# Performance work log

Hardware: AMD Instinct MI355X
Metric: run time of the kernel (lower is better)

Reference implementation:

```python
import jax, jax.numpy as jnp
import numpy as np

H, DK = 8, 32
D_MODEL = H * DK  # 256
Q_DIM = K_DIM = V_DIM = 256
B, T, S = 4, 4, 1024
NEG = -1e10


def setup_inputs() -> dict:
    rng = jax.random.key(0)
    ks = jax.random.split(rng, 12)
    w = lambda k, shp: (jax.random.normal(k, shp, jnp.float32) * 0.02)
    return {
        "query": jax.random.normal(ks[0], (B, T, S, Q_DIM), jnp.float32),
        "key": jax.random.normal(ks[1], (B, T, S, K_DIM), jnp.float32),
        "value": jax.random.normal(ks[2], (B, T, S, V_DIM), jnp.float32),
        "mask": jax.random.randint(ks[3], (B, T), 1, S + 1),  # valid lengths in [1, S]
        "Wq": w(ks[4], (D_MODEL, Q_DIM)), "bq": jnp.zeros((D_MODEL,), jnp.float32),
        "Wk": w(ks[5], (D_MODEL, K_DIM)), "bk": jnp.zeros((D_MODEL,), jnp.float32),
        "Wv": w(ks[6], (D_MODEL, V_DIM)), "bv": jnp.zeros((D_MODEL,), jnp.float32),
        "Wo": w(ks[7], (Q_DIM, D_MODEL)), "bo": jnp.zeros((Q_DIM,), jnp.float32),
    }


def reference(query, key, value, mask, Wq, bq, Wk, bk, Wv, bv, Wo, bo):
    b, t, s, _ = query.shape
    # projections -> [B,T,h,S,d_k]
    def proj(x, W, bias):
        y = jnp.einsum('btsf,df->btsd', x, W) + bias
        return y.reshape(b, t, s, H, DK).transpose(0, 1, 3, 2, 4)
    q = proj(query, Wq, bq)
    k = proj(key, Wk, bk)
    v = proj(value, Wv, bv)
    # scores [B,T,h,S,S]
    scores = jnp.einsum('bthqd,bthkd->bthqk', q, k) / jnp.sqrt(jnp.float32(DK))
    # vectorized length mask: positions < len on both axes (replaces torch python loop)
    valid = jnp.arange(s)[None, None, :] < mask[:, :, None]        # [B,T,S]
    m = valid[:, :, None, :, None] & valid[:, :, None, None, :]    # [B,T,1,S,S]
    scores = jnp.where(m, scores, NEG)
    p = jax.nn.softmax(scores, axis=-1)
    x = jnp.einsum('bthqk,bthkd->bthqd', p, v)                     # [B,T,h,S,d_k]
    x = x.transpose(0, 1, 3, 2, 4).reshape(b, t, s, H * DK)
    return jnp.einsum('btsd,qd->btsq', x, Wo) + bo
```

## Files before the change

kernel.cpp:

```cpp
#include <hip/hip_runtime.h>

#define EXPC 0.25505654442163f

typedef __attribute__((ext_vector_type(8))) short bfrag;
typedef __attribute__((ext_vector_type(4))) float ffrag;
typedef __attribute__((ext_vector_type(8))) unsigned int u8v;
typedef __attribute__((ext_vector_type(4))) unsigned int u4v;
typedef __attribute__((ext_vector_type(2))) unsigned int u2v;

__device__ __forceinline__ short f2bf(float x) {
  union { float f; unsigned u; } v; v.f = x;
  return (short)((v.u + 0x8000u) >> 16);
}

__device__ __forceinline__ unsigned int packbf(float a, float b) {
  return __builtin_amdgcn_perm(__float_as_uint(b) + 0x8000u,
                               __float_as_uint(a) + 0x8000u, 0x07060302u);
}

__device__ __forceinline__ bfrag cvtp(u8v x) {
  u4v r;
#pragma unroll
  for (int i = 0; i < 4; ++i)
    r[i] = __builtin_amdgcn_perm(x[2 * i + 1] + 0x8000u, x[2 * i] + 0x8000u, 0x07060302u);
  union { u4v u; bfrag b; } c; c.u = r; return c.b;
}
__device__ __forceinline__ bfrag cvt8(const float* __restrict__ p) {
  return cvtp(*(const u8v*)p);
}

__global__ __launch_bounds__(256, 4) void proj_kv(
    const float* __restrict__ kin, const float* __restrict__ Wk,
    const float* __restrict__ bk, const float* __restrict__ vin,
    const float* __restrict__ Wv, const float* __restrict__ bv,
    short* __restrict__ ko, short* __restrict__ vt) {
  const int t = threadIdx.x;
  const int lane = t & 63, wid = t >> 6;
  const int lrow = lane & 15, lq = lane >> 4;
  __shared__ __align__(16) char lds[18432];
  const int row4 = t >> 2, c4 = (t & 3) * 8;

  const bool isK = blockIdx.x < 512;
  if (isK) {
    const int bx = blockIdx.x >> 1, d0 = (blockIdx.x & 1) * 128;
    const int m0 = bx * 64;
    short* Ab = (short*)lds;
    short* Bb = (short*)(lds + 5120);
    short* tile = (short*)lds;
    ffrag acc[4][2] = {};
    u8v pa, pb0, pb1;
    pa  = *(const u8v*)(kin + (size_t)(m0 + row4) * 256 + c4);
    pb0 = *(const u8v*)(Wk + (size_t)(d0 + row4) * 256 + c4);
    pb1 = *(const u8v*)(Wk + (size_t)(d0 + 64 + row4) * 256 + c4);
    *(bfrag*)(Ab + row4 * 40 + c4) = cvtp(pa);
    *(bfrag*)(Bb + row4 * 40 + c4) = cvtp(pb0);
    *(bfrag*)(Bb + (64 + row4) * 40 + c4) = cvtp(pb1);
#pragma unroll 1
    for (int s = 0; s < 8; ++s) {
      __syncthreads();
      if (s < 7) {
        const int k1 = (s + 1) * 32;
        pa  = *(const u8v*)(kin + (size_t)(m0 + row4) * 256 + k1 + c4);
        pb0 = *(const u8v*)(Wk + (size_t)(d0 + row4) * 256 + k1 + c4);
        pb1 = *(const u8v*)(Wk + (size_t)(d0 + 64 + row4) * 256 + k1 + c4);
      }
      bfrag a[4], b[2];
#pragma unroll
      for (int i = 0; i < 4; ++i)
        a[i] = *(const bfrag*)(Ab + (i * 16 + lrow) * 40 + lq * 8);
#pragma unroll
      for (int j = 0; j < 2; ++j)
        b[j] = *(const bfrag*)(Bb + (wid * 32 + j * 16 + lrow) * 40 + lq * 8);
#pragma unroll
      for (int i = 0; i < 4; ++i)
#pragma unroll
        for (int j = 0; j < 2; ++j)
          acc[i][j] = __builtin_amdgcn_mfma_f32_16x16x32_bf16(a[i], b[j], acc[i][j], 0, 0, 0);
      __syncthreads();
      if (s < 7) {
        *(bfrag*)(Ab + row4 * 40 + c4) = cvtp(pa);
        *(bfrag*)(Bb + row4 * 40 + c4) = cvtp(pb0);
        *(bfrag*)(Bb + (64 + row4) * 40 + c4) = cvtp(pb1);
      }
    }
    __syncthreads();
#pragma unroll
    for (int j = 0; j < 2; ++j) {
      int dl = wid * 32 + j * 16 + lrow;
      float bs = bk[d0 + dl];
#pragma unroll
      for (int i = 0; i < 4; ++i)
#pragma unroll
        for (int r = 0; r < 4; ++r)
          tile[(i * 16 + lq * 4 + r) * 136 + dl] = f2bf(acc[i][j][r] + bs);
    }
    __syncthreads();
#pragma unroll
    for (int p = 0; p < 4; ++p) {
      int id2 = p * 256 + t;
      int row = id2 >> 4, c = id2 & 15;
      bfrag v = *(const bfrag*)(tile + row * 136 + c * 8);
      *(bfrag*)(ko + (size_t)(m0 + row) * 256 + d0 + c * 8) = v;
    }
  } else {
    const int t2 = blockIdx.x - 512;
    const int bx = t2 >> 1, d0 = (t2 & 1) * 128;
    const int n0 = bx * 64;
    short* Aw = (short*)lds;
    short* Bv = (short*)(lds + 10240);
    short* tile = (short*)lds;
    ffrag acc[2][4] = {};
    u8v pv, pw0, pw1;
    pw0 = *(const u8v*)(Wv + (size_t)(d0 + row4) * 256 + c4);
    pw1 = *(const u8v*)(Wv + (size_t)(d0 + 64 + row4) * 256 + c4);
    pv  = *(const u8v*)(vin + (size_t)(n0 + row4) * 256 + c4);
    *(bfrag*)(Aw + row4 * 40 + c4) = cvtp(pw0);
    *(bfrag*)(Aw + (64 + row4) * 40 + c4) = cvtp(pw1);
    *(bfrag*)(Bv + row4 * 40 + c4) = cvtp(pv);
#pragma unroll 1
    for (int s = 0; s < 8; ++s) {
      __syncthreads();
      if (s < 7) {
        const int k1 = (s + 1) * 32;
        pw0 = *(const u8v*)(Wv + (size_t)(d0 + row4) * 256 + k1 + c4);
        pw1 = *(const u8v*)(Wv + (size_t)(d0 + 64 + row4) * 256 + k1 + c4);
        pv  = *(const u8v*)(vin + (size_t)(n0 + row4) * 256 + k1 + c4);
      }
      bfrag a[2], b[4];
#pragma unroll
      for (int i = 0; i < 2; ++i)
        a[i] = *(const bfrag*)(Aw + (wid * 32 + i * 16 + lrow) * 40 + lq * 8);
#pragma unroll
      for (int j = 0; j < 4; ++j)
        b[j] = *(const bfrag*)(Bv + (j * 16 + lrow) * 40 + lq * 8);
#pragma unroll
      for (int i = 0; i < 2; ++i)
#pragma unroll
        for (int j = 0; j < 4; ++j)
          acc[i][j] = __builtin_amdgcn_mfma_f32_16x16x32_bf16(a[i], b[j], acc[i][j], 0, 0, 0);
      __syncthreads();
      if (s < 7) {
        *(bfrag*)(Aw + row4 * 40 + c4) = cvtp(pw0);
        *(bfrag*)(Aw + (64 + row4) * 40 + c4) = cvtp(pw1);
        *(bfrag*)(Bv + row4 * 40 + c4) = cvtp(pv);
      }
    }
    __syncthreads();
#pragma unroll
    for (int i = 0; i < 2; ++i)
#pragma unroll
      for (int r = 0; r < 4; ++r) {
        int dl = wid * 32 + i * 16 + lq * 4 + r;
        float bs = bv[d0 + dl];
#pragma unroll
        for (int j = 0; j < 4; ++j)
          tile[dl * 72 + j * 16 + lrow] = f2bf(acc[i][j][r] + bs);
      }
    __syncthreads();
    const int bt = n0 >> 10, sl0 = n0 & 1023;
#pragma unroll
    for (int p = 0; p < 4; ++p) {
      int id2 = p * 256 + t;
      int dl = id2 >> 3, c = id2 & 7;
      bfrag v = *(const bfrag*)(tile + dl * 72 + c * 8);
      *(bfrag*)(vt + (size_t)bt * 262144 + (size_t)(d0 + dl) * 1024 + sl0 + c * 8) = v;
    }
  }
}

__global__ __launch_bounds__(512, 4) void attn_fused(
    const float* __restrict__ query, const float* __restrict__ Wq,
    const float* __restrict__ bq, const float* __restrict__ Wo,
    const float* __restrict__ bo, const short* __restrict__ K,
    const short* __restrict__ Vt, const int* __restrict__ mask,
    float* __restrict__ out) {
  const int lane = threadIdx.x & 63, wid = threadIdx.x >> 6;
  const int lrow = lane & 15, lq = lane >> 4;
  const int id = blockIdx.x;
  const int bt = (id + (id >> 8)) & 15;
  const int qt = id >> 4;
  const int q0 = qt * 32;
  const int L = mask[bt];
  const int h = wid;
  const bool isLast = (qt == 31);
  const int nvalid = min(max(L - q0, 0), 32);

  if (nvalid <= 0 && !isLast) return;
  const bool colsumOnly = isLast && (nvalid <= 0);

  __shared__ __align__(16) short qx[32 * 264];
  __shared__ __align__(16) unsigned int ptbuf[8][16 * 36];
  unsigned int* ptg = &ptbuf[wid][0];
  float* vbuf = (float*)&ptbuf[0][0];

  const short* Vb = Vt + ((size_t)bt * 8 + h) * 32768;
  float l_i[2];
  ffrag o[2][2] = {};

  if (!colsumOnly) {
    {
      const int n0 = h * 32;
      const float* X = query + ((size_t)bt * 1024 + q0) * 256;
      ffrag acc[2][2] = {};
      u8v xa[2], wb[2], xa_n[2], wb_n[2];
#pragma unroll
      for (int i = 0; i < 2; ++i)
        xa[i] = *(const u8v*)(X + (size_t)(i * 16 + lrow) * 256 + lq * 8);
#pragma unroll
      for (int j = 0; j < 2; ++j)
        wb[j] = *(const u8v*)(Wq + (size_t)(n0 + j * 16 + lrow) * 256 + lq * 8);
#pragma unroll 1
      for (int tt = 0; tt < 8; ++tt) {
        if (tt < 7) {
          const int kk = (tt + 1) * 32;
#pragma unroll
          for (int i = 0; i < 2; ++i)
            xa_n[i] = *(const u8v*)(X + (size_t)(i * 16 + lrow) * 256 + kk + lq * 8);
#pragma unroll
          for (int j = 0; j < 2; ++j)
            wb_n[j] = *(const u8v*)(Wq + (size_t)(n0 + j * 16 + lrow) * 256 + kk + lq * 8);
        }
        bfrag a[2], b[2];
#pragma unroll
        for (int i = 0; i < 2; ++i) a[i] = cvtp(xa[i]);
#pragma unroll
        for (int j = 0; j < 2; ++j) b[j] = cvtp(wb[j]);
#pragma unroll
        for (int i = 0; i < 2; ++i)
#pragma unroll
          for (int j = 0; j < 2; ++j)
            acc[i][j] = __builtin_amdgcn_mfma_f32_16x16x32_bf16(a[i], b[j], acc[i][j], 0, 0, 0);
#pragma unroll
        for (int i = 0; i < 2; ++i) xa[i] = xa_n[i];
#pragma unroll
        for (int j = 0; j < 2; ++j) wb[j] = wb_n[j];
      }
#pragma unroll
      for (int j = 0; j < 2; ++j) {
        int d = n0 + j * 16 + lrow;
        float bs = bq[d];
#pragma unroll
        for (int i = 0; i < 2; ++i)
#pragma unroll
          for (int r = 0; r < 4; ++r)
            qx[(i * 16 + lq * 4 + r) * 264 + d] = f2bf((acc[i][j][r] + bs) * EXPC);
      }
    }

    const short* Kb = K + (size_t)bt * 262144;
    bfrag qf[2];
#pragma unroll
    for (int g = 0; g < 2; ++g)
      qf[g] = *(const bfrag*)(qx + (g * 16 + lrow) * 264 + h * 32 + lq * 8);

    const int nchunk = (L + 63) >> 6;
    float l_loc[2] = {0.f, 0.f};
    bfrag kf[4], kf_n[4];
#pragma unroll
    for (int f = 0; f < 4; ++f)
      kf[f] = *(const bfrag*)(Kb + (size_t)(f * 16 + lrow) * 256 + h * 32 + lq * 8);

#pragma unroll 1
    for (int c = 0; c < nchunk; ++c) {
      const int kc = c * 64;
      const ffrag zf = {0.f, 0.f, 0.f, 0.f};
      if (c + 1 < nchunk) {
#pragma unroll
        for (int f = 0; f < 4; ++f)
          kf_n[f] = *(const bfrag*)(Kb + (size_t)(kc + 64 + f * 16 + lrow) * 256 + h * 32 + lq * 8);
      }
      bfrag av[2][2];
#pragma unroll
      for (int dj = 0; dj < 2; ++dj)
#pragma unroll
        for (int b = 0; b < 2; ++b)
          av[dj][b] = *(const bfrag*)(Vb + (size_t)(dj * 16 + lrow) * 1024 + kc + b * 32 + lq * 8);

      ffrag st[2][4];
#pragma unroll
      for (int g = 0; g < 2; ++g)
#pragma unroll
        for (int f = 0; f < 4; ++f)
          st[g][f] = __builtin_amdgcn_mfma_f32_16x16x32_bf16(kf[f], qf[g], zf, 0, 0, 0);

      const bool fullc = (kc + 64 <= L);
#pragma unroll
      for (int g = 0; g < 2; ++g) {
        float p[4][4];
        if (fullc) {
#pragma unroll
          for (int f = 0; f < 4; ++f)
#pragma unroll
            for (int r = 0; r < 4; ++r) {
              p[f][r] = __builtin_amdgcn_exp2f(st[g][f][r]);
              l_loc[g] += p[f][r];
            }
        } else {
#pragma unroll
          for (int f = 0; f < 4; ++f)
#pragma unroll
            for (int r = 0; r < 4; ++r) {
              int kr = kc + f * 16 + lq * 4 + r;
              float pv = (kr < L) ? __builtin_amdgcn_exp2f(st[g][f][r]) : 0.f;
              p[f][r] = pv;
              l_loc[g] += pv;
            }
        }
#pragma unroll
        for (int f = 0; f < 4; ++f) {
          u2v w;
          w[0] = packbf(p[f][0], p[f][1]);
          w[1] = packbf(p[f][2], p[f][3]);
          *(u2v*)(ptg + lrow * 36 + 8 * f + 2 * lq) = w;
        }
#pragma unroll
        for (int b = 0; b < 2; ++b) {
          u4v pv = *(const u4v*)(ptg + lrow * 36 + 16 * b + 4 * lq);
          union { u4v u; bfrag bf; } pt; pt.u = pv;
#pragma unroll
          for (int dj = 0; dj < 2; ++dj)
            o[g][dj] = __builtin_amdgcn_mfma_f32_16x16x32_bf16(av[dj][b], pt.bf, o[g][dj], 0, 0, 0);
        }
      }
#pragma unroll
      for (int f = 0; f < 4; ++f) kf[f] = kf_n[f];
    }

#pragma unroll
    for (int g = 0; g < 2; ++g) {
      float rs = l_loc[g];
      rs += __shfl_xor(rs, 16);
      rs += __shfl_xor(rs, 32);
      l_i[g] = rs;
    }
  } else {
#pragma unroll
    for (int g = 0; g < 2; ++g) l_i[g] = 1024.f;
  }

  if (isLast && nvalid < 32) {
#pragma unroll
    for (int g = 0; g < 2; ++g) {
      bool inv = (g * 16 + lrow) >= nvalid;
      if (inv) {
        l_i[g] = 1024.f;
#pragma unroll
        for (int dj = 0; dj < 2; ++dj)
#pragma unroll
          for (int r = 0; r < 4; ++r) o[g][dj][r] = 0.f;
      }
    }
    bfrag ind[2];
#pragma unroll
    for (int g = 0; g < 2; ++g) {
      short iv = ((g * 16 + lrow) >= nvalid) ? (short)0x3F80 : (short)0;
#pragma unroll
      for (int j = 0; j < 8; ++j) ind[g][j] = iv;
    }
    const bool g0 = (nvalid < 16);
#pragma unroll 2
    for (int kc = 0; kc < 1024; kc += 64) {
#pragma unroll
      for (int dj = 0; dj < 2; ++dj)
#pragma unroll
        for (int b = 0; b < 2; ++b) {
          bfrag av = *(const bfrag*)(Vb + (size_t)(dj * 16 + lrow) * 1024 + kc + b * 32 + lq * 8);
          if (g0)
            o[0][dj] = __builtin_amdgcn_mfma_f32_16x16x32_bf16(av, ind[0], o[0][dj], 0, 0, 0);
          o[1][dj] = __builtin_amdgcn_mfma_f32_16x16x32_bf16(av, ind[1], o[1][dj], 0, 0, 0);
        }
    }
  }

#pragma unroll
  for (int g = 0; g < 2; ++g) {
    float rcp = 1.0f / l_i[g];
#pragma unroll
    for (int dj = 0; dj < 2; ++dj) {
      u2v w;
      w[0] = packbf(o[g][dj][0] * rcp, o[g][dj][1] * rcp);
      w[1] = packbf(o[g][dj][2] * rcp, o[g][dj][3] * rcp);
      short* dst = qx + (g * 16 + lrow) * 264 + h * 32 + dj * 16 + lq * 4;
      *(u2v*)dst = w;
    }
  }
  __syncthreads();

  {
    const int n0 = h * 32;
    ffrag acc[2][2] = {};
    u8v wb[2], wb_n[2];
#pragma unroll
    for (int j = 0; j < 2; ++j)
      wb[j] = *(const u8v*)(Wo + (size_t)(n0 + j * 16 + lrow) * 256 + lq * 8);
#pragma unroll 1
    for (int tt = 0; tt < 8; ++tt) {
      const int k0 = tt * 32;
      if (tt < 7) {
#pragma unroll
        for (int j = 0; j < 2; ++j)
          wb_n[j] = *(const u8v*)(Wo + (size_t)(n0 + j * 16 + lrow) * 256 + k0 + 32 + lq * 8);
      }
      bfrag a[2], b[2];
#pragma unroll
      for (int i = 0; i < 2; ++i)
        a[i] = *(const bfrag*)(qx + (i * 16 + lrow) * 264 + k0 + lq * 8);
#pragma unroll
      for (int j = 0; j < 2; ++j) b[j] = cvtp(wb[j]);
#pragma unroll
      for (int i = 0; i < 2; ++i)
#pragma unroll
        for (int j = 0; j < 2; ++j)
          acc[i][j] = __builtin_amdgcn_mfma_f32_16x16x32_bf16(a[i], b[j], acc[i][j], 0, 0, 0);
#pragma unroll
      for (int j = 0; j < 2; ++j) wb[j] = wb_n[j];
    }

    if (!colsumOnly) {
#pragma unroll
      for (int j = 0; j < 2; ++j) {
        int d = n0 + j * 16 + lrow;
        float bs = bo[d];
#pragma unroll
        for (int i = 0; i < 2; ++i)
#pragma unroll
          for (int r = 0; r < 4; ++r) {
            int qr = q0 + i * 16 + lq * 4 + r;
            if (qr < L || isLast)
              out[((size_t)bt * 1024 + qr) * 256 + d] = acc[i][j][r] + bs;
          }
      }
    } else {
      if (lq == 0) {
#pragma unroll
        for (int j = 0; j < 2; ++j) {
          int d = n0 + j * 16 + lrow;
          vbuf[d] = acc[0][j][0] + bo[d];
        }
      }
      __syncthreads();
      const int d = threadIdx.x & 255;
      const float vv = vbuf[d];
      float* ob = out + (size_t)bt * 1024 * 256 + d;
#pragma unroll 1
      for (int row = L + (threadIdx.x >> 8); row < 1024; row += 2)
        ob[(size_t)row * 256] = vv;
    }
  }
}

extern "C" void kernel_launch(void* const* d_in, const int* in_sizes, int n_in,
                              void* d_out, int out_size, void* d_ws, size_t ws_size,
                              hipStream_t stream) {
  const float* query = (const float*)d_in[0];
  const float* key   = (const float*)d_in[1];
  const float* value = (const float*)d_in[2];
  const int*   mask  = (const int*)d_in[3];
  const float* Wq = (const float*)d_in[4];
  const float* bq = (const float*)d_in[5];
  const float* Wk = (const float*)d_in[6];
  const float* bk = (const float*)d_in[7];
  const float* Wv = (const float*)d_in[8];
  const float* bv = (const float*)d_in[9];
  const float* Wo = (const float*)d_in[10];
  const float* bo = (const float*)d_in[11];
  float* out = (float*)d_out;

  short* k_ws  = (short*)d_ws;
  short* vt_ws = k_ws + 4194304;

  proj_kv<<<dim3(1024), 256, 0, stream>>>(key, Wk, bk, value, Wv, bv, k_ws, vt_ws);
  attn_fused<<<dim3(512), 512, 0, stream>>>(query, Wq, bq, Wo, bo,
                                            k_ws, vt_ws, mask, out);
}
```

Baseline: 207.2 us.

## Split each 32-row query tile into two 16-row blocks and prefetch V

```diff
diff --git a/kernel.cpp b/kernel.cpp
--- a/kernel.cpp
+++ b/kernel.cpp
@@ -177,35 +177,37 @@
   const int lane = threadIdx.x & 63, wid = threadIdx.x >> 6;
   const int lrow = lane & 15, lq = lane >> 4;
   const int id = blockIdx.x;
-  const int bt = (id + (id >> 8)) & 15;
-  const int qt = id >> 4;
+  const int qt = id >> 5;
+  const int bt = (((id >> 1) & 15) + (id >> 9)) & 15;
+  const int g = id & 1;
   const int q0 = qt * 32;
   const int L = mask[bt];
   const int h = wid;
   const bool isLast = (qt == 31);
   const int nvalid = min(max(L - q0, 0), 32);
-
-  if (nvalid <= 0 && !isLast) return;
-  const bool colsumOnly = isLast && (nvalid <= 0);
-
-  __shared__ __align__(16) short qx[32 * 264];
+  const int gn = nvalid - g * 16;
+
+  if (gn <= 0 && !isLast) return;
+  const bool dmode = isLast && (nvalid <= 0);
+  if (dmode && g == 1) return;
+  const bool skip12 = isLast && (gn <= 0);
+
+  __shared__ __align__(16) short qx[16 * 264];
   __shared__ __align__(16) unsigned int ptbuf[8][16 * 36];
   unsigned int* ptg = &ptbuf[wid][0];
   float* vbuf = (float*)&ptbuf[0][0];
 
   const short* Vb = Vt + ((size_t)bt * 8 + h) * 32768;
-  float l_i[2];
-  ffrag o[2][2] = {};
-
-  if (!colsumOnly) {
+  float l_i;
+  ffrag o[2] = {};
+
+  if (!skip12) {
     {
       const int n0 = h * 32;
-      const float* X = query + ((size_t)bt * 1024 + q0) * 256;
-      ffrag acc[2][2] = {};
-      u8v xa[2], wb[2], xa_n[2], wb_n[2];
-#pragma unroll
-      for (int i = 0; i < 2; ++i)
-        xa[i] = *(const u8v*)(X + (size_t)(i * 16 + lrow) * 256 + lq * 8);
+      const float* X = query + ((size_t)bt * 1024 + q0 + g * 16) * 256;
+      ffrag acc[2] = {};
+      u8v xa, wb[2], xa_n, wb_n[2];
+      xa = *(const u8v*)(X + (size_t)lrow * 256 + lq * 8);
 #pragma unroll
       for (int j = 0; j < 2; ++j)
         wb[j] = *(const u8v*)(Wq + (size_t)(n0 + j * 16 + lrow) * 256 + lq * 8);
@@ -213,25 +215,18 @@
       for (int tt = 0; tt < 8; ++tt) {
         if (tt < 7) {
           const int kk = (tt + 1) * 32;
-#pragma unroll
-          for (int i = 0; i < 2; ++i)
-            xa_n[i] = *(const u8v*)(X + (size_t)(i * 16 + lrow) * 256 + kk + lq * 8);
+          xa_n = *(const u8v*)(X + (size_t)lrow * 256 + kk + lq * 8);
 #pragma unroll
           for (int j = 0; j < 2; ++j)
             wb_n[j] = *(const u8v*)(Wq + (size_t)(n0 + j * 16 + lrow) * 256 + kk + lq * 8);
         }
-        bfrag a[2], b[2];
-#pragma unroll
-        for (int i = 0; i < 2; ++i) a[i] = cvtp(xa[i]);
-#pragma unroll
-        for (int j = 0; j < 2; ++j) b[j] = cvtp(wb[j]);
-#pragma unroll
-        for (int i = 0; i < 2; ++i)
-#pragma unroll
-          for (int j = 0; j < 2; ++j)
-            acc[i][j] = __builtin_amdgcn_mfma_f32_16x16x32_bf16(a[i], b[j], acc[i][j], 0, 0, 0);
-#pragma unroll
-        for (int i = 0; i < 2; ++i) xa[i] = xa_n[i];
+        bfrag a = cvtp(xa);
+#pragma unroll
+        for (int j = 0; j < 2; ++j) {
+          bfrag b = cvtp(wb[j]);
+          acc[j] = __builtin_amdgcn_mfma_f32_16x16x32_bf16(a, b, acc[j], 0, 0, 0);
+        }
+        xa = xa_n;
 #pragma unroll
         for (int j = 0; j < 2; ++j) wb[j] = wb_n[j];
       }
@@ -240,25 +235,24 @@
         int d = n0 + j * 16 + lrow;
         float bs = bq[d];
 #pragma unroll
-        for (int i = 0; i < 2; ++i)
-#pragma unroll
-          for (int r = 0; r < 4; ++r)
-            qx[(i * 16 + lq * 4 + r) * 264 + d] = f2bf((acc[i][j][r] + bs) * EXPC);
+        for (int r = 0; r < 4; ++r)
+          qx[(lq * 4 + r) * 264 + d] = f2bf((acc[j][r] + bs) * EXPC);
       }
     }
 
     const short* Kb = K + (size_t)bt * 262144;
-    bfrag qf[2];
-#pragma unroll
-    for (int g = 0; g < 2; ++g)
-      qf[g] = *(const bfrag*)(qx + (g * 16 + lrow) * 264 + h * 32 + lq * 8);
-
+    bfrag qf = *(const bfrag*)(qx + lrow * 264 + h * 32 + lq * 8);
     const int nchunk = (L + 63) >> 6;
-    float l_loc[2] = {0.f, 0.f};
-    bfrag kf[4], kf_n[4];
+    float l_loc = 0.f;
+    bfrag kf[4], kf_n[4], av[2][2], av_n[2][2];
 #pragma unroll
     for (int f = 0; f < 4; ++f)
       kf[f] = *(const bfrag*)(Kb + (size_t)(f * 16 + lrow) * 256 + h * 32 + lq * 8);
+#pragma unroll
+    for (int dj = 0; dj < 2; ++dj)
+#pragma unroll
+      for (int b = 0; b < 2; ++b)
+        av[dj][b] = *(const bfrag*)(Vb + (size_t)(dj * 16 + lrow) * 1024 + b * 32 + lq * 8);
 
 #pragma unroll 1
     for (int c = 0; c < nchunk; ++c) {
@@ -268,127 +262,113 @@
 #pragma unroll
         for (int f = 0; f < 4; ++f)
           kf_n[f] = *(const bfrag*)(Kb + (size_t)(kc + 64 + f * 16 + lrow) * 256 + h * 32 + lq * 8);
-      }
-      bfrag av[2][2];
+#pragma unroll
+        for (int dj = 0; dj < 2; ++dj)
+#pragma unroll
+          for (int b = 0; b < 2; ++b)
+            av_n[dj][b] = *(const bfrag*)(Vb + (size_t)(dj * 16 + lrow) * 1024 + kc + 64 + b * 32 + lq * 8);
+      }
+      ffrag st[4];
+#pragma unroll
+      for (int f = 0; f < 4; ++f)
+        st[f] = __builtin_amdgcn_mfma_f32_16x16x32_bf16(kf[f], qf, zf, 0, 0, 0);
+
+      float p[4][4];
+      const bool fullc = (kc + 64 <= L);
+      if (fullc) {
+#pragma unroll
+        for (int f = 0; f < 4; ++f)
+#pragma unroll
+          for (int r = 0; r < 4; ++r) {
+            p[f][r] = __builtin_amdgcn_exp2f(st[f][r]);
+            l_loc += p[f][r];
+          }
+      } else {
+#pragma unroll
+        for (int f = 0; f < 4; ++f)
+#pragma unroll
+          for (int r = 0; r < 4; ++r) {
+            int kr = kc + f * 16 + lq * 4 + r;
+            float pv = (kr < L) ? __builtin_amdgcn_exp2f(st[f][r]) : 0.f;
+            p[f][r] = pv;
+            l_loc += pv;
+          }
+      }
+#pragma unroll
+      for (int f = 0; f < 4; ++f) {
+        u2v w;
+        w[0] = packbf(p[f][0], p[f][1]);
+        w[1] = packbf(p[f][2], p[f][3]);
+        *(u2v*)(ptg + lrow * 36 + 8 * f + 2 * lq) = w;
+      }
+#pragma unroll
+      for (int b = 0; b < 2; ++b) {
+        u4v pv = *(const u4v*)(ptg + lrow * 36 + 16 * b + 4 * lq);
+        union { u4v u; bfrag bf; } pt; pt.u = pv;
+#pragma unroll
+        for (int dj = 0; dj < 2; ++dj)
+          o[dj] = __builtin_amdgcn_mfma_f32_16x16x32_bf16(av[dj][b], pt.bf, o[dj], 0, 0, 0);
+      }
+#pragma unroll
+      for (int f = 0; f < 4; ++f) kf[f] = kf_n[f];
 #pragma unroll
       for (int dj = 0; dj < 2; ++dj)
 #pragma unroll
-        for (int b = 0; b < 2; ++b)
-          av[dj][b] = *(const bfrag*)(Vb + (size_t)(dj * 16 + lrow) * 1024 + kc + b * 32 + lq * 8);
-
-      ffrag st[2][4];
-#pragma unroll
-      for (int g = 0; g < 2; ++g)
-#pragma unroll
-        for (int f = 0; f < 4; ++f)
-          st[g][f] = __builtin_amdgcn_mfma_f32_16x16x32_bf16(kf[f], qf[g], zf, 0, 0, 0);
-
-      const bool fullc = (kc + 64 <= L);
-#pragma unroll
-      for (int g = 0; g < 2; ++g) {
-        float p[4][4];
-        if (fullc) {
-#pragma unroll
-          for (int f = 0; f < 4; ++f)
-#pragma unroll
-            for (int r = 0; r < 4; ++r) {
-              p[f][r] = __builtin_amdgcn_exp2f(st[g][f][r]);
-              l_loc[g] += p[f][r];
-            }
-        } else {
-#pragma unroll
-          for (int f = 0; f < 4; ++f)
-#pragma unroll
-            for (int r = 0; r < 4; ++r) {
-              int kr = kc + f * 16 + lq * 4 + r;
-              float pv = (kr < L) ? __builtin_amdgcn_exp2f(st[g][f][r]) : 0.f;
-              p[f][r] = pv;
-              l_loc[g] += pv;
-            }
-        }
-#pragma unroll
-        for (int f = 0; f < 4; ++f) {
-          u2v w;
-          w[0] = packbf(p[f][0], p[f][1]);
-          w[1] = packbf(p[f][2], p[f][3]);
-          *(u2v*)(ptg + lrow * 36 + 8 * f + 2 * lq) = w;
-        }
-#pragma unroll
-        for (int b = 0; b < 2; ++b) {
-          u4v pv = *(const u4v*)(ptg + lrow * 36 + 16 * b + 4 * lq);
-          union { u4v u; bfrag bf; } pt; pt.u = pv;
-#pragma unroll
-          for (int dj = 0; dj < 2; ++dj)
-            o[g][dj] = __builtin_amdgcn_mfma_f32_16x16x32_bf16(av[dj][b], pt.bf, o[g][dj], 0, 0, 0);
-        }
-      }
-#pragma unroll
-      for (int f = 0; f < 4; ++f) kf[f] = kf_n[f];
-    }
-
-#pragma unroll
-    for (int g = 0; g < 2; ++g) {
-      float rs = l_loc[g];
+        for (int b = 0; b < 2; ++b) av[dj][b] = av_n[dj][b];
+    }
+
+    {
+      float rs = l_loc;
       rs += __shfl_xor(rs, 16);
       rs += __shfl_xor(rs, 32);
-      l_i[g] = rs;
+      l_i = rs;
     }
   } else {
-#pragma unroll
-    for (int g = 0; g < 2; ++g) l_i[g] = 1024.f;
+    l_i = 1024.f;
   }
 
-  if (isLast && nvalid < 32) {
-#pragma unroll
-    for (int g = 0; g < 2; ++g) {
-      bool inv = (g * 16 + lrow) >= nvalid;
-      if (inv) {
-        l_i[g] = 1024.f;
-#pragma unroll
-        for (int dj = 0; dj < 2; ++dj)
-#pragma unroll
-          for (int r = 0; r < 4; ++r) o[g][dj][r] = 0.f;
-      }
-    }
-    bfrag ind[2];
-#pragma unroll
-    for (int g = 0; g < 2; ++g) {
-      short iv = ((g * 16 + lrow) >= nvalid) ? (short)0x3F80 : (short)0;
-#pragma unroll
-      for (int j = 0; j < 8; ++j) ind[g][j] = iv;
-    }
-    const bool g0 = (nvalid < 16);
+  if (isLast && gn < 16) {
+    const bool inv = (lrow >= gn);
+    if (inv) {
+      l_i = 1024.f;
+#pragma unroll
+      for (int dj = 0; dj < 2; ++dj)
+#pragma unroll
+        for (int r = 0; r < 4; ++r) o[dj][r] = 0.f;
+    }
+    bfrag ind;
+    {
+      short iv = inv ? (short)0x3F80 : (short)0;
+#pragma unroll
+      for (int j = 0; j < 8; ++j) ind[j] = iv;
+    }
 #pragma unroll 2
     for (int kc = 0; kc < 1024; kc += 64) {
 #pragma unroll
       for (int dj = 0; dj < 2; ++dj)
 #pragma unroll
         for (int b = 0; b < 2; ++b) {
-          bfrag av = *(const bfrag*)(Vb + (size_t)(dj * 16 + lrow) * 1024 + kc + b * 32 + lq * 8);
-          if (g0)
-            o[0][dj] = __builtin_amdgcn_mfma_f32_16x16x32_bf16(av, ind[0], o[0][dj], 0, 0, 0);
-          o[1][dj] = __builtin_amdgcn_mfma_f32_16x16x32_bf16(av, ind[1], o[1][dj], 0, 0, 0);
+          bfrag avt = *(const bfrag*)(Vb + (size_t)(dj * 16 + lrow) * 1024 + kc + b * 32 + lq * 8);
+          o[dj] = __builtin_amdgcn_mfma_f32_16x16x32_bf16(avt, ind, o[dj], 0, 0, 0);
         }
     }
   }
 
-#pragma unroll
-  for (int g = 0; g < 2; ++g) {
-    float rcp = 1.0f / l_i[g];
+  {
+    const float rcp = 1.0f / l_i;
 #pragma unroll
     for (int dj = 0; dj < 2; ++dj) {
       u2v w;
-      w[0] = packbf(o[g][dj][0] * rcp, o[g][dj][1] * rcp);
-      w[1] = packbf(o[g][dj][2] * rcp, o[g][dj][3] * rcp);
-      short* dst = qx + (g * 16 + lrow) * 264 + h * 32 + dj * 16 + lq * 4;
-      *(u2v*)dst = w;
+      w[0] = packbf(o[dj][0] * rcp, o[dj][1] * rcp);
+      w[1] = packbf(o[dj][2] * rcp, o[dj][3] * rcp);
+      *(u2v*)(qx + lrow * 264 + h * 32 + dj * 16 + lq * 4) = w;
     }
   }
   __syncthreads();
 
   {
     const int n0 = h * 32;
-    ffrag acc[2][2] = {};
+    ffrag acc[2] = {};
     u8v wb[2], wb_n[2];
 #pragma unroll
     for (int j = 0; j < 2; ++j)
@@ -401,41 +381,34 @@
         for (int j = 0; j < 2; ++j)
           wb_n[j] = *(const u8v*)(Wo + (size_t)(n0 + j * 16 + lrow) * 256 + k0 + 32 + lq * 8);
       }
-      bfrag a[2], b[2];
-#pragma unroll
-      for (int i = 0; i < 2; ++i)
-        a[i] = *(const bfrag*)(qx + (i * 16 + lrow) * 264 + k0 + lq * 8);
-#pragma unroll
-      for (int j = 0; j < 2; ++j) b[j] = cvtp(wb[j]);
-#pragma unroll
-      for (int i = 0; i < 2; ++i)
-#pragma unroll
-        for (int j = 0; j < 2; ++j)
-          acc[i][j] = __builtin_amdgcn_mfma_f32_16x16x32_bf16(a[i], b[j], acc[i][j], 0, 0, 0);
+      bfrag a = *(const bfrag*)(qx + lrow * 264 + k0 + lq * 8);
+#pragma unroll
+      for (int j = 0; j < 2; ++j) {
+        bfrag b = cvtp(wb[j]);
+        acc[j] = __builtin_amdgcn_mfma_f32_16x16x32_bf16(a, b, acc[j], 0, 0, 0);
+      }
 #pragma unroll
       for (int j = 0; j < 2; ++j) wb[j] = wb_n[j];
     }
 
-    if (!colsumOnly) {
+    if (!dmode) {
 #pragma unroll
       for (int j = 0; j < 2; ++j) {
         int d = n0 + j * 16 + lrow;
         float bs = bo[d];
 #pragma unroll
-        for (int i = 0; i < 2; ++i)
-#pragma unroll
-          for (int r = 0; r < 4; ++r) {
-            int qr = q0 + i * 16 + lq * 4 + r;
-            if (qr < L || isLast)
-              out[((size_t)bt * 1024 + qr) * 256 + d] = acc[i][j][r] + bs;
-          }
+        for (int r = 0; r < 4; ++r) {
+          int qr = q0 + g * 16 + lq * 4 + r;
+          if (qr < L || isLast)
+            out[((size_t)bt * 1024 + qr) * 256 + d] = acc[j][r] + bs;
+        }
       }
     } else {
       if (lq == 0) {
 #pragma unroll
         for (int j = 0; j < 2; ++j) {
           int d = n0 + j * 16 + lrow;
-          vbuf[d] = acc[0][j][0] + bo[d];
+          vbuf[d] = acc[j][0] + bo[d];
         }
       }
       __syncthreads();
@@ -470,6 +443,6 @@
   short* vt_ws = k_ws + 4194304;
 
   proj_kv<<<dim3(1024), 256, 0, stream>>>(key, Wk, bk, value, Wv, bv, k_ws, vt_ws);
-  attn_fused<<<dim3(512), 512, 0, stream>>>(query, Wq, bq, Wo, bo,
-                                            k_ws, vt_ws, mask, out);
-}
+  attn_fused<<<dim3(1024), 512, 0, stream>>>(query, Wq, bq, Wo, bo,
+                                             k_ws, vt_ws, mask, out);
+}
```

New measurement: 265.3 us. 1.28x slower.

## Double-buffer K and V loads with inline asm and explicit waitcnt

Applied to the files above, without the earlier changes.

```diff
diff --git a/kernel.cpp b/kernel.cpp
--- a/kernel.cpp
+++ b/kernel.cpp
@@ -24,9 +24,6 @@
   for (int i = 0; i < 4; ++i)
     r[i] = __builtin_amdgcn_perm(x[2 * i + 1] + 0x8000u, x[2 * i] + 0x8000u, 0x07060302u);
   union { u4v u; bfrag b; } c; c.u = r; return c.b;
-}
-__device__ __forceinline__ bfrag cvt8(const float* __restrict__ p) {
-  return cvtp(*(const u8v*)p);
 }
 
 __global__ __launch_bounds__(256, 4) void proj_kv(
@@ -168,7 +165,70 @@
   }
 }
 
-__global__ __launch_bounds__(512, 4) void attn_fused(
+#define ISSUE(kf_, av_, kc1)                                                     \
+  do {                                                                           \
+    _Pragma("unroll") for (int f_ = 0; f_ < 4; ++f_) {                           \
+      const short* pk_ = Kb + (size_t)((kc1) + f_ * 16 + lrow) * 256 + h * 32 + lq * 8; \
+      asm volatile("global_load_dwordx4 %0, %1, off" : "=v"(kf_[f_]) : "v"(pk_)); \
+    }                                                                            \
+    _Pragma("unroll") for (int dj_ = 0; dj_ < 2; ++dj_)                          \
+      _Pragma("unroll") for (int b_ = 0; b_ < 2; ++b_) {                         \
+        const short* pv_ = Vb + (size_t)(dj_ * 16 + lrow) * 1024 + (kc1) + b_ * 32 + lq * 8; \
+        asm volatile("global_load_dwordx4 %0, %1, off" : "=v"(av_[dj_][b_]) : "v"(pv_)); \
+      }                                                                          \
+  } while (0)
+
+#define WAITP(kf_, av_)                                                          \
+  do {                                                                           \
+    asm volatile("s_waitcnt vmcnt(0)"                                            \
+                 : "+v"(kf_[0]), "+v"(kf_[1]), "+v"(kf_[2]), "+v"(kf_[3]),       \
+                   "+v"(av_[0][0]), "+v"(av_[0][1]), "+v"(av_[1][0]), "+v"(av_[1][1]) \
+                 :: "memory");                                                   \
+    __builtin_amdgcn_sched_barrier(0);                                           \
+  } while (0)
+
+#define PCHUNK(kf_, av_, kcv)                                                    \
+  do {                                                                           \
+    const int kc_ = (kcv);                                                       \
+    const ffrag zf_ = {0.f, 0.f, 0.f, 0.f};                                      \
+    ffrag st_[2][4];                                                             \
+    _Pragma("unroll") for (int g_ = 0; g_ < 2; ++g_)                             \
+      _Pragma("unroll") for (int f_ = 0; f_ < 4; ++f_)                           \
+        st_[g_][f_] = __builtin_amdgcn_mfma_f32_16x16x32_bf16(kf_[f_], qf[g_], zf_, 0, 0, 0); \
+    const bool fullc_ = (kc_ + 64 <= L);                                         \
+    _Pragma("unroll") for (int g_ = 0; g_ < 2; ++g_) {                           \
+      float p_[4][4];                                                            \
+      if (fullc_) {                                                              \
+        _Pragma("unroll") for (int f_ = 0; f_ < 4; ++f_)                         \
+          _Pragma("unroll") for (int r_ = 0; r_ < 4; ++r_) {                     \
+            p_[f_][r_] = __builtin_amdgcn_exp2f(st_[g_][f_][r_]);                \
+            l_loc[g_] += p_[f_][r_];                                             \
+          }                                                                      \
+      } else {                                                                   \
+        _Pragma("unroll") for (int f_ = 0; f_ < 4; ++f_)                         \
+          _Pragma("unroll") for (int r_ = 0; r_ < 4; ++r_) {                     \
+            int kr_ = kc_ + f_ * 16 + lq * 4 + r_;                               \
+            float pvx_ = (kr_ < L) ? __builtin_amdgcn_exp2f(st_[g_][f_][r_]) : 0.f; \
+            p_[f_][r_] = pvx_;                                                   \
+            l_loc[g_] += pvx_;                                                   \
+          }                                                                      \
+      }                                                                          \
+      _Pragma("unroll") for (int f_ = 0; f_ < 4; ++f_) {                         \
+        u2v w_;                                                                  \
+        w_[0] = packbf(p_[f_][0], p_[f_][1]);                                    \
+        w_[1] = packbf(p_[f_][2], p_[f_][3]);                                    \
+        *(u2v*)(ptg + lrow * 36 + 8 * f_ + 2 * lq) = w_;                         \
+      }                                                                          \
+      _Pragma("unroll") for (int b_ = 0; b_ < 2; ++b_) {                         \
+        u4v pv4_ = *(const u4v*)(ptg + lrow * 36 + 16 * b_ + 4 * lq);            \
+        union { u4v u; bfrag bf; } pt_; pt_.u = pv4_;                            \
+        _Pragma("unroll") for (int dj_ = 0; dj_ < 2; ++dj_)                      \
+          o[g_][dj_] = __builtin_amdgcn_mfma_f32_16x16x32_bf16(av_[dj_][b_], pt_.bf, o[g_][dj_], 0, 0, 0); \
+      }                                                                          \
+    }                                                                            \
+  } while (0)
+
+__global__ __launch_bounds__(512, 2) void attn_fused(
     const float* __restrict__ query, const float* __restrict__ Wq,
     const float* __restrict__ bq, const float* __restrict__ Wo,
     const float* __restrict__ bo, const short* __restrict__ K,
@@ -255,75 +315,19 @@
 
     const int nchunk = (L + 63) >> 6;
     float l_loc[2] = {0.f, 0.f};
-    bfrag kf[4], kf_n[4];
-#pragma unroll
-    for (int f = 0; f < 4; ++f)
-      kf[f] = *(const bfrag*)(Kb + (size_t)(f * 16 + lrow) * 256 + h * 32 + lq * 8);
-
-#pragma unroll 1
-    for (int c = 0; c < nchunk; ++c) {
-      const int kc = c * 64;
-      const ffrag zf = {0.f, 0.f, 0.f, 0.f};
-      if (c + 1 < nchunk) {
-#pragma unroll
-        for (int f = 0; f < 4; ++f)
-          kf_n[f] = *(const bfrag*)(Kb + (size_t)(kc + 64 + f * 16 + lrow) * 256 + h * 32 + lq * 8);
-      }
-      bfrag av[2][2];
-#pragma unroll
-      for (int dj = 0; dj < 2; ++dj)
-#pragma unroll
-        for (int b = 0; b < 2; ++b)
-          av[dj][b] = *(const bfrag*)(Vb + (size_t)(dj * 16 + lrow) * 1024 + kc + b * 32 + lq * 8);
-
-      ffrag st[2][4];
-#pragma unroll
-      for (int g = 0; g < 2; ++g)
-#pragma unroll
-        for (int f = 0; f < 4; ++f)
-          st[g][f] = __builtin_amdgcn_mfma_f32_16x16x32_bf16(kf[f], qf[g], zf, 0, 0, 0);
-
-      const bool fullc = (kc + 64 <= L);
-#pragma unroll
-      for (int g = 0; g < 2; ++g) {
-        float p[4][4];
-        if (fullc) {
-#pragma unroll
-          for (int f = 0; f < 4; ++f)
-#pragma unroll
-            for (int r = 0; r < 4; ++r) {
-              p[f][r] = __builtin_amdgcn_exp2f(st[g][f][r]);
-              l_loc[g] += p[f][r];
-            }
-        } else {
-#pragma unroll
-          for (int f = 0; f < 4; ++f)
-#pragma unroll
-            for (int r = 0; r < 4; ++r) {
-              int kr = kc + f * 16 + lq * 4 + r;
-              float pv = (kr < L) ? __builtin_amdgcn_exp2f(st[g][f][r]) : 0.f;
-              p[f][r] = pv;
-              l_loc[g] += pv;
-            }
-        }
-#pragma unroll
-        for (int f = 0; f < 4; ++f) {
-          u2v w;
-          w[0] = packbf(p[f][0], p[f][1]);
-          w[1] = packbf(p[f][2], p[f][3]);
-          *(u2v*)(ptg + lrow * 36 + 8 * f + 2 * lq) = w;
-        }
-#pragma unroll
-        for (int b = 0; b < 2; ++b) {
-          u4v pv = *(const u4v*)(ptg + lrow * 36 + 16 * b + 4 * lq);
-          union { u4v u; bfrag bf; } pt; pt.u = pv;
-#pragma unroll
-          for (int dj = 0; dj < 2; ++dj)
-            o[g][dj] = __builtin_amdgcn_mfma_f32_16x16x32_bf16(av[dj][b], pt.bf, o[g][dj], 0, 0, 0);
-        }
-      }
-#pragma unroll
-      for (int f = 0; f < 4; ++f) kf[f] = kf_n[f];
+    bfrag kfA[4] = {}, avA[2][2] = {}, kfB[4] = {}, avB[2][2] = {};
+
+    int c = 0;
+    ISSUE(kfA, avA, 0);
+    for (;;) {
+      WAITP(kfA, avA);
+      if (c + 1 < nchunk) ISSUE(kfB, avB, (c + 1) * 64);
+      PCHUNK(kfA, avA, c * 64);
+      if (++c >= nchunk) break;
+      WAITP(kfB, avB);
+      if (c + 1 < nchunk) ISSUE(kfA, avA, (c + 1) * 64);
+      PCHUNK(kfB, avB, c * 64);
+      if (++c >= nchunk) break;
     }
 
 #pragma unroll
```

Result: no change. 207.6 us (+0.2%).
